# Kernel tuning notes

Hardware: AMD Instinct MI355X
Metric: run time of the kernel (lower is better)

## Reference

```python
import jax, jax.numpy as jnp
import numpy as np


def _binarize_ste(w):
    # forward: sign(w) in {-1, +1}; backward: identity (straight-through)
    wb = jnp.where(w >= 0, 1.0, -1.0).astype(w.dtype)
    return w + jax.lax.stop_gradient(wb - w)


def setup_inputs() -> dict:
    key = jax.random.key(0)
    k1, k2 = jax.random.split(key)
    IN, OUT, N = 2048, 2048, 8192
    x = jax.random.normal(k1, (N, IN), dtype=jnp.float32)
    # kaiming_uniform-like init: U(-bound, bound), bound = sqrt(6/in)*? (gain sqrt(5) default in torch)
    bound = float(np.sqrt(6.0 / IN))
    weight = jax.random.uniform(k2, (OUT, IN), dtype=jnp.float32, minval=-bound, maxval=bound)
    bias = jnp.zeros((OUT,), dtype=jnp.float32)
    return {"x": x, "weight": weight, "bias": bias}


def reference(x, weight, bias):
    w_binary = _binarize_ste(weight)  # [out, in], values in {-1, +1}
    # F.linear: x @ W^T + b
    return jnp.einsum('ni,oi->no', x, w_binary) + bias
```

## Files before the change

### kernel.cpp

```cpp
#include <hip/hip_runtime.h>
#include <stdint.h>


typedef __bf16 bf16x8 __attribute__((ext_vector_type(8)));
typedef float f32x16 __attribute__((ext_vector_type(16)));

typedef const __attribute__((address_space(1))) void* gas_ptr;
typedef __attribute__((address_space(3))) void* lds_ptr;

__device__ __forceinline__ unsigned short f2bf_rne(float f) {
    unsigned int u = __builtin_bit_cast(unsigned int, f);
    u += 0x7fffu + ((u >> 16) & 1u);
    return (unsigned short)(u >> 16);
}

__global__ __launch_bounds__(256) void cvt_x_kernel(const float* __restrict__ in,
                                                    unsigned short* __restrict__ out,
                                                    int n8) {
    int i = blockIdx.x * 256 + threadIdx.x;
    if (i >= n8) return;
    const float4* p = reinterpret_cast<const float4*>(in + (size_t)i * 8);
    float4 f0 = p[0], f1 = p[1];
    union { unsigned short s[8]; uint4 v; } o;
    o.s[0] = f2bf_rne(f0.x); o.s[1] = f2bf_rne(f0.y);
    o.s[2] = f2bf_rne(f0.z); o.s[3] = f2bf_rne(f0.w);
    o.s[4] = f2bf_rne(f1.x); o.s[5] = f2bf_rne(f1.y);
    o.s[6] = f2bf_rne(f1.z); o.s[7] = f2bf_rne(f1.w);
    *reinterpret_cast<uint4*>(out + (size_t)i * 8) = o.v;
}

__global__ __launch_bounds__(256) void bin_w_kernel(const float* __restrict__ in,
                                                    unsigned short* __restrict__ out,
                                                    int n4) {
    int i = blockIdx.x * 256 + threadIdx.x;
    if (i >= n4) return;
    float4 f = reinterpret_cast<const float4*>(in)[i];
    union { unsigned short s[4]; uint2 v; } o;
    o.s[0] = (f.x >= 0.f) ? 0x3F80u : 0xBF80u;
    o.s[1] = (f.y >= 0.f) ? 0x3F80u : 0xBF80u;
    o.s[2] = (f.z >= 0.f) ? 0x3F80u : 0xBF80u;
    o.s[3] = (f.w >= 0.f) ? 0x3F80u : 0xBF80u;
    reinterpret_cast<uint2*>(out)[i] = o.v;
}


#define WAITVM(N) asm volatile("s_waitcnt vmcnt(" #N ")" ::: "memory")

__device__ __forceinline__ void block_bar() {
    asm volatile("" ::: "memory");
    __builtin_amdgcn_s_barrier();
    asm volatile("" ::: "memory");
}

__global__ __launch_bounds__(512, 2) void gemm_bin_kernel(
    const unsigned short* __restrict__ A,
    const unsigned short* __restrict__ B,
    const float* __restrict__ bias,
    float* __restrict__ C,
    int M, int N, int K)
{
    __shared__ __align__(16) unsigned char smem_raw[131072];
    unsigned short* const sm = (unsigned short*)smem_raw;

    const int tid  = threadIdx.x;
    const int lane = tid & 63;
    const int wave = tid >> 6;
    const int wm   = wave >> 2;
    const int wn   = wave & 3;
    const int bm   = blockIdx.y;
    const int bn   = blockIdx.x;

    const unsigned short* __restrict__ Agb = A + (size_t)(bm * 256) * K;
    const unsigned short* __restrict__ Bgb = B + (size_t)(bn * 256) * K;

    const int lr = lane & 31;
    const int lk = lane >> 5;

    int offA[4][2], offB[2][2];
#pragma unroll
    for (int m = 0; m < 4; ++m) {
        const int r = wm * 128 + m * 32 + lr;
#pragma unroll
        for (int ks = 0; ks < 2; ++ks) {
            const int c = ks * 2 + lk;
            offA[m][ks] = (r * 4 + (c ^ ((r >> 1) & 3))) * 8;
        }
    }
#pragma unroll
    for (int n = 0; n < 2; ++n) {
        const int r = wn * 64 + n * 32 + lr;
#pragma unroll
        for (int ks = 0; ks < 2; ++ks) {
            const int c = ks * 2 + lk;
            offB[n][ks] = (r * 4 + (c ^ ((r >> 1) & 3))) * 8;
        }
    }

    int goff[2], lso[2];
#pragma unroll
    for (int j = 0; j < 2; ++j) {
        const int g = j * 512 + tid;
        const int r = g >> 2;
        const int c = (g & 3) ^ ((r >> 1) & 3);
        goff[j] = r * K + c * 8;
        lso[j]  = g * 8;
    }

    f32x16 acc[4][2];
#pragma unroll
    for (int m = 0; m < 4; ++m)
#pragma unroll
        for (int n = 0; n < 2; ++n)
#pragma unroll
            for (int r = 0; r < 16; ++r) acc[m][n][r] = 0.f;

    const int KT = K >> 5;

    auto stage = [&](int ts) {
        unsigned short* lA = sm + (ts & 3) * 16384;
        unsigned short* lB = lA + 8192;
        const unsigned short* ga = Agb + (size_t)ts * 32;
        const unsigned short* gb = Bgb + (size_t)ts * 32;
        __builtin_amdgcn_global_load_lds((gas_ptr)(ga + goff[0]), (lds_ptr)(lA + lso[0]), 16, 0, 0);
        __builtin_amdgcn_global_load_lds((gas_ptr)(ga + goff[1]), (lds_ptr)(lA + lso[1]), 16, 0, 0);
        __builtin_amdgcn_global_load_lds((gas_ptr)(gb + goff[0]), (lds_ptr)(lB + lso[0]), 16, 0, 0);
        __builtin_amdgcn_global_load_lds((gas_ptr)(gb + goff[1]), (lds_ptr)(lB + lso[1]), 16, 0, 0);
    };

    auto compute = [&](int t) {
        const unsigned short* lA = sm + (t & 3) * 16384;
        const unsigned short* lB = lA + 8192;
        bf16x8 af[4][2], bf[2][2];
#pragma unroll
        for (int m = 0; m < 4; ++m)
#pragma unroll
            for (int ks = 0; ks < 2; ++ks)
                af[m][ks] = *reinterpret_cast<const bf16x8*>(lA + offA[m][ks]);
#pragma unroll
        for (int n = 0; n < 2; ++n)
#pragma unroll
            for (int ks = 0; ks < 2; ++ks)
                bf[n][ks] = *reinterpret_cast<const bf16x8*>(lB + offB[n][ks]);
        __builtin_amdgcn_s_setprio(1);
#pragma unroll
        for (int ks = 0; ks < 2; ++ks)
#pragma unroll
            for (int m = 0; m < 4; ++m)
#pragma unroll
                for (int n = 0; n < 2; ++n)
                    acc[m][n] = __builtin_amdgcn_mfma_f32_32x32x16_bf16(
                        af[m][ks], bf[n][ks], acc[m][n], 0, 0, 0);
        __builtin_amdgcn_s_setprio(0);
    };

    stage(0); stage(1); stage(2);

    int t = 0;
    for (; t < KT - 3; ++t) {
        stage(t + 3);
        WAITVM(12);
        block_bar();
        compute(t);
        block_bar();
    }
    WAITVM(8);  block_bar(); compute(t); block_bar(); ++t;
    WAITVM(4);  block_bar(); compute(t); block_bar(); ++t;
    WAITVM(0);  block_bar(); compute(t);

    const int colb = bn * 256 + wn * 64;
    const float bv0 = bias[colb + lr];
    const float bv1 = bias[colb + 32 + lr];
    const int r0 = bm * 256 + wm * 128 + 4 * lk;
#pragma unroll
    for (int m = 0; m < 4; ++m)
#pragma unroll
        for (int n = 0; n < 2; ++n) {
            const float bvn = n ? bv1 : bv0;
            float* cp = C + (size_t)(r0 + m * 32) * N + colb + n * 32 + lr;
#pragma unroll
            for (int r = 0; r < 16; ++r) {
                const int rr = (r & 3) + 8 * (r >> 2);
                cp[(size_t)rr * N] = acc[m][n][r] + bvn;
            }
        }
}

extern "C" void kernel_launch(void* const* d_in, const int* in_sizes, int n_in,
                              void* d_out, int out_size, void* d_ws, size_t ws_size,
                              hipStream_t stream) {
    const float* x    = (const float*)d_in[0];
    const float* w    = (const float*)d_in[1];
    const float* bias = (const float*)d_in[2];
    float* out = (float*)d_out;

    const int K = 2048;
    const int N = in_sizes[2];
    const int M = in_sizes[0] / K;

    unsigned short* xb = (unsigned short*)d_ws;
    unsigned short* wb = xb + (size_t)M * K;

    const int nx8 = (M * K) / 8;
    const int nw4 = (N * K) / 4;
    cvt_x_kernel<<<(nx8 + 255) / 256, 256, 0, stream>>>(x, xb, nx8);
    bin_w_kernel<<<(nw4 + 255) / 256, 256, 0, stream>>>(w, wb, nw4);

    dim3 grid(N / 256, M / 256);
    gemm_bin_kernel<<<grid, 512, 0, stream>>>(xb, wb, bias, out, M, N, K);
}
```

Before: 201.3 us.

## Restructure GEMM main loop into four-phase ping-pong with interleaved staging

Replaces the 4-deep single-K-tile pipeline with a 64-wide K tile split into two 32-wide halves across double buffers. Each iteration runs four phases that each issue global-to-LDS loads for a future half-tile, read LDS fragments, sync, and run a batch of MFMAs, so memory traffic is spread across the compute. The bias load is hoisted before the loop. This adds more barriers per K step and more complex wait-count bookkeeping, which risks stalls or race bugs if the counts are wrong.

```diff
diff --git a/kernel.cpp b/kernel.cpp
--- a/kernel.cpp
+++ b/kernel.cpp
@@ -43,7 +43,6 @@
     reinterpret_cast<uint2*>(out)[i] = o.v;
 }
 
-
 #define WAITVM(N) asm volatile("s_waitcnt vmcnt(" #N ")" ::: "memory")
 
 __device__ __forceinline__ void block_bar() {
@@ -73,27 +72,32 @@
     const unsigned short* __restrict__ Agb = A + (size_t)(bm * 256) * K;
     const unsigned short* __restrict__ Bgb = B + (size_t)(bn * 256) * K;
 
-    const int lr = lane & 31;
-    const int lk = lane >> 5;
-
-    int offA[4][2], offB[2][2];
-#pragma unroll
-    for (int m = 0; m < 4; ++m) {
-        const int r = wm * 128 + m * 32 + lr;
-#pragma unroll
-        for (int ks = 0; ks < 2; ++ks) {
-            const int c = ks * 2 + lk;
-            offA[m][ks] = (r * 4 + (c ^ ((r >> 1) & 3))) * 8;
+    const int lr   = lane & 31;
+    const int lkhi = lane >> 5;
+
+    int offA[2][2][2][2];
+    int offB[2][2][2];
+#pragma unroll
+    for (int mh = 0; mh < 2; ++mh)
+#pragma unroll
+        for (int mi = 0; mi < 2; ++mi) {
+            const int r = wm * 128 + mh * 64 + mi * 32 + lr;
+            const int s = (r >> 1) & 3;
+#pragma unroll
+            for (int kh = 0; kh < 2; ++kh)
+#pragma unroll
+                for (int kk = 0; kk < 2; ++kk)
+                    offA[mh][mi][kh][kk] = kh * 8192 + (r * 4 + ((kk * 2 + lkhi) ^ s)) * 8;
         }
-    }
-#pragma unroll
-    for (int n = 0; n < 2; ++n) {
-        const int r = wn * 64 + n * 32 + lr;
-#pragma unroll
-        for (int ks = 0; ks < 2; ++ks) {
-            const int c = ks * 2 + lk;
-            offB[n][ks] = (r * 4 + (c ^ ((r >> 1) & 3))) * 8;
-        }
+#pragma unroll
+    for (int ni = 0; ni < 2; ++ni) {
+        const int r = wn * 64 + ni * 32 + lr;
+        const int s = (r >> 1) & 3;
+#pragma unroll
+        for (int kh = 0; kh < 2; ++kh)
+#pragma unroll
+            for (int kk = 0; kk < 2; ++kk)
+                offB[ni][kh][kk] = 16384 + kh * 8192 + (r * 4 + ((kk * 2 + lkhi) ^ s)) * 8;
     }
 
     int goff[2], lso[2];
@@ -106,6 +110,11 @@
         lso[j]  = g * 8;
     }
 
+    const int colb = bn * 256 + wn * 64;
+    float bv0 = bias[colb + lr];
+    float bv1 = bias[colb + 32 + lr];
+    asm volatile("" :: "v"(bv0), "v"(bv1));
+
     f32x16 acc[4][2];
 #pragma unroll
     for (int m = 0; m < 4; ++m)
@@ -114,63 +123,92 @@
 #pragma unroll
             for (int r = 0; r < 16; ++r) acc[m][n][r] = 0.f;
 
-    const int KT = K >> 5;
-
-    auto stage = [&](int ts) {
-        unsigned short* lA = sm + (ts & 3) * 16384;
-        unsigned short* lB = lA + 8192;
-        const unsigned short* ga = Agb + (size_t)ts * 32;
-        const unsigned short* gb = Bgb + (size_t)ts * 32;
-        __builtin_amdgcn_global_load_lds((gas_ptr)(ga + goff[0]), (lds_ptr)(lA + lso[0]), 16, 0, 0);
-        __builtin_amdgcn_global_load_lds((gas_ptr)(ga + goff[1]), (lds_ptr)(lA + lso[1]), 16, 0, 0);
-        __builtin_amdgcn_global_load_lds((gas_ptr)(gb + goff[0]), (lds_ptr)(lB + lso[0]), 16, 0, 0);
-        __builtin_amdgcn_global_load_lds((gas_ptr)(gb + goff[1]), (lds_ptr)(lB + lso[1]), 16, 0, 0);
+    bf16x8 bfr[2][2];
+
+    auto stage2 = [&](const unsigned short* gsrc, int ldsoff) {
+#pragma unroll
+        for (int j = 0; j < 2; ++j)
+            __builtin_amdgcn_global_load_lds((gas_ptr)(gsrc + goff[j]),
+                                             (lds_ptr)(sm + ldsoff + lso[j]), 16, 0, 0);
     };
 
-    auto compute = [&](int t) {
-        const unsigned short* lA = sm + (t & 3) * 16384;
-        const unsigned short* lB = lA + 8192;
-        bf16x8 af[4][2], bf[2][2];
-#pragma unroll
-        for (int m = 0; m < 4; ++m)
-#pragma unroll
-            for (int ks = 0; ks < 2; ++ks)
-                af[m][ks] = *reinterpret_cast<const bf16x8*>(lA + offA[m][ks]);
-#pragma unroll
-        for (int n = 0; n < 2; ++n)
-#pragma unroll
-            for (int ks = 0; ks < 2; ++ks)
-                bf[n][ks] = *reinterpret_cast<const bf16x8*>(lB + offB[n][ks]);
+    auto phase = [&](int bb, int mh, int kh, int readB,
+                     const unsigned short* gsrc, int ldsoff, int dostage) {
+        if (readB) {
+#pragma unroll
+            for (int ni = 0; ni < 2; ++ni)
+#pragma unroll
+                for (int kk = 0; kk < 2; ++kk)
+                    bfr[ni][kk] = *reinterpret_cast<const bf16x8*>(
+                        sm + bb + offB[ni][kh][kk]);
+        }
+        bf16x8 af[2][2];
+#pragma unroll
+        for (int mi = 0; mi < 2; ++mi)
+#pragma unroll
+            for (int kk = 0; kk < 2; ++kk)
+                af[mi][kk] = *reinterpret_cast<const bf16x8*>(
+                    sm + bb + offA[mh][mi][kh][kk]);
+        if (dostage) stage2(gsrc, ldsoff);
+        block_bar();
+        asm volatile("s_waitcnt lgkmcnt(0)" ::: "memory");
+        __builtin_amdgcn_sched_barrier(0);
         __builtin_amdgcn_s_setprio(1);
 #pragma unroll
-        for (int ks = 0; ks < 2; ++ks)
-#pragma unroll
-            for (int m = 0; m < 4; ++m)
-#pragma unroll
-                for (int n = 0; n < 2; ++n)
-                    acc[m][n] = __builtin_amdgcn_mfma_f32_32x32x16_bf16(
-                        af[m][ks], bf[n][ks], acc[m][n], 0, 0, 0);
+        for (int kk = 0; kk < 2; ++kk)
+#pragma unroll
+            for (int mi = 0; mi < 2; ++mi)
+#pragma unroll
+                for (int ni = 0; ni < 2; ++ni)
+                    acc[mh * 2 + mi][ni] = __builtin_amdgcn_mfma_f32_32x32x16_bf16(
+                        af[mi][kk], bfr[ni][kk], acc[mh * 2 + mi][ni], 0, 0, 0);
+        __builtin_amdgcn_sched_barrier(0);
         __builtin_amdgcn_s_setprio(0);
     };
 
-    stage(0); stage(1); stage(2);
-
-    int t = 0;
-    for (; t < KT - 3; ++t) {
-        stage(t + 3);
-        WAITVM(12);
-        block_bar();
-        compute(t);
-        block_bar();
-    }
-    WAITVM(8);  block_bar(); compute(t); block_bar(); ++t;
-    WAITVM(4);  block_bar(); compute(t); block_bar(); ++t;
-    WAITVM(0);  block_bar(); compute(t);
-
-    const int colb = bn * 256 + wn * 64;
-    const float bv0 = bias[colb + lr];
-    const float bv1 = bias[colb + 32 + lr];
-    const int r0 = bm * 256 + wm * 128 + 4 * lk;
+    const int KT = K >> 6;
+
+    stage2(Agb,      0);
+    stage2(Bgb,      16384);
+    stage2(Agb + 32, 8192);
+    stage2(Bgb + 32, 24576);
+    stage2(Agb + 64, 32768);
+    stage2(Bgb + 64, 32768 + 16384);
+    WAITVM(8);
+    block_bar();
+
+    for (int T = 0; T < KT - 2; ++T) {
+        const int bb = (T & 1) << 15;
+        const int nb = bb ^ 32768;
+        const unsigned short* gA1 = Agb + (size_t)(T + 1) * 64 + 32;
+        const unsigned short* gB1 = Bgb + (size_t)(T + 1) * 64 + 32;
+        const unsigned short* gA0 = Agb + (size_t)(T + 2) * 64;
+        const unsigned short* gB0 = Bgb + (size_t)(T + 2) * 64;
+        phase(bb, 0, 0, 1, gA1, nb + 8192,  1);            block_bar();
+        phase(bb, 1, 0, 0, gB1, nb + 24576, 1); WAITVM(8); block_bar();
+        phase(bb, 0, 1, 1, gA0, bb,         1);            block_bar();
+        phase(bb, 1, 1, 0, gB0, bb + 16384, 1); WAITVM(8); block_bar();
+    }
+    {
+        const int bb = ((KT - 2) & 1) << 15;
+        const int nb = bb ^ 32768;
+        const unsigned short* gA1 = Agb + (size_t)(KT - 1) * 64 + 32;
+        const unsigned short* gB1 = Bgb + (size_t)(KT - 1) * 64 + 32;
+        phase(bb, 0, 0, 1, gA1, nb + 8192,  1);            block_bar();
+        phase(bb, 1, 0, 0, gB1, nb + 24576, 1); WAITVM(8); block_bar();
+        phase(bb, 0, 1, 1, Agb, 0,          0);            block_bar();
+        phase(bb, 1, 1, 0, Agb, 0,          0); WAITVM(4); block_bar();
+    }
+    {
+        const int bb = ((KT - 1) & 1) << 15;
+        phase(bb, 0, 0, 1, Agb, 0, 0);                     block_bar();
+        phase(bb, 1, 0, 0, Agb, 0, 0);          WAITVM(0); block_bar();
+        phase(bb, 0, 1, 1, Agb, 0, 0);                     block_bar();
+        phase(bb, 1, 1, 0, Agb, 0, 0);
+    }
+
+    const float* bvp = bias;  (void)bvp;
+    const int r0 = bm * 256 + wm * 128 + 4 * lkhi;
 #pragma unroll
     for (int m = 0; m < 4; ++m)
 #pragma unroll
```

Result: faster. 193.4 us (-3.9%).

## Restructure bf16 GEMM main loop to 16x16x32 MFMA with double-buffered K=64 tiles

Applied to the files above, without the earlier changes.

Replaces the 32x32x16 MFMA tiling with 16x16x32 MFMAs (8x4 fragments per wave) and changes the LDS staging from a 4-deep ring of K=32 tiles to a double buffer of K=64 tiles with a new swizzle. The next tile's global-to-LDS loads are issued at the start of each K step and waited on at its end. Each K step is split into four M-subphases separated by block barriers, with explicit lgkmcnt waits and sched barriers around the MFMA bursts. The aim is fewer loop iterations and a different LDS access pattern, but it brings more barriers per step and shallower prefetch than the 3-ahead pipeline it replaces.

```diff
diff --git a/kernel.cpp b/kernel.cpp
--- a/kernel.cpp
+++ b/kernel.cpp
@@ -3,7 +3,7 @@
 
 
 typedef __bf16 bf16x8 __attribute__((ext_vector_type(8)));
-typedef float f32x16 __attribute__((ext_vector_type(16)));
+typedef float f32x4 __attribute__((ext_vector_type(4)));
 
 typedef const __attribute__((address_space(1))) void* gas_ptr;
 typedef __attribute__((address_space(3))) void* lds_ptr;
@@ -43,7 +43,6 @@
     reinterpret_cast<uint2*>(out)[i] = o.v;
 }
 
-
 #define WAITVM(N) asm volatile("s_waitcnt vmcnt(" #N ")" ::: "memory")
 
 __device__ __forceinline__ void block_bar() {
@@ -73,115 +72,118 @@
     const unsigned short* __restrict__ Agb = A + (size_t)(bm * 256) * K;
     const unsigned short* __restrict__ Bgb = B + (size_t)(bn * 256) * K;
 
-    const int lr = lane & 31;
-    const int lk = lane >> 5;
-
-    int offA[4][2], offB[2][2];
-#pragma unroll
-    for (int m = 0; m < 4; ++m) {
-        const int r = wm * 128 + m * 32 + lr;
-#pragma unroll
-        for (int ks = 0; ks < 2; ++ks) {
-            const int c = ks * 2 + lk;
-            offA[m][ks] = (r * 4 + (c ^ ((r >> 1) & 3))) * 8;
+    const int r15 = lane & 15;
+    const int kc  = lane >> 4;
+    const int sw  = ((r15 >> 2) & 1) << 1;
+
+    const int baseA0 = wm * 8192 + r15 * 64 + ((kc    ) ^ sw) * 8;
+    const int baseA1 = wm * 8192 + r15 * 64 + ((kc + 4) ^ sw) * 8;
+    const int bBq    = 16384 + (wn >> 1) * 8192 + (wn & 1) * 4096 + r15 * 64;
+    const int baseB0 = bBq + ((kc    ) ^ sw) * 8;
+    const int baseB1 = bBq + ((kc + 4) ^ sw) * 8;
+
+    int gsoff[2], ldoff[2];
+#pragma unroll
+    for (int j = 0; j < 2; ++j) {
+        const int g  = j * 512 + tid;
+        const int rl = g >> 3;
+        const int c  = (g & 7) ^ (((rl >> 2) & 1) << 1);
+        gsoff[j] = rl * K + c * 8;
+        ldoff[j] = g * 8;
+    }
+
+    const int colb = bn * 256 + wn * 64;
+    float bv[4];
+#pragma unroll
+    for (int nf = 0; nf < 4; ++nf) {
+        bv[nf] = bias[colb + nf * 16 + r15];
+        asm volatile("" :: "v"(bv[nf]));
+    }
+
+    f32x4 acc[8][4];
+#pragma unroll
+    for (int m = 0; m < 8; ++m)
+#pragma unroll
+        for (int n = 0; n < 4; ++n)
+#pragma unroll
+            for (int r = 0; r < 4; ++r) acc[m][n][r] = 0.f;
+
+    bf16x8 bfr[4][2];
+
+    auto stageAll = [&](int T1, unsigned short* dst) {
+        const unsigned short* ga = Agb + (size_t)T1 * 64;
+        const unsigned short* gb = Bgb + (size_t)T1 * 64;
+#pragma unroll
+        for (int j = 0; j < 2; ++j)
+            __builtin_amdgcn_global_load_lds((gas_ptr)(ga + gsoff[j]),
+                                             (lds_ptr)(dst + ldoff[j]), 16, 0, 0);
+#pragma unroll
+        for (int j = 0; j < 2; ++j)
+            __builtin_amdgcn_global_load_lds((gas_ptr)(ga + (size_t)128 * K + gsoff[j]),
+                                             (lds_ptr)(dst + 8192 + ldoff[j]), 16, 0, 0);
+#pragma unroll
+        for (int j = 0; j < 2; ++j)
+            __builtin_amdgcn_global_load_lds((gas_ptr)(gb + gsoff[j]),
+                                             (lds_ptr)(dst + 16384 + ldoff[j]), 16, 0, 0);
+#pragma unroll
+        for (int j = 0; j < 2; ++j)
+            __builtin_amdgcn_global_load_lds((gas_ptr)(gb + (size_t)128 * K + gsoff[j]),
+                                             (lds_ptr)(dst + 24576 + ldoff[j]), 16, 0, 0);
+    };
+
+    const int KT = K >> 6;
+
+    stageAll(0, sm);
+    WAITVM(0);
+    block_bar();
+
+    for (int T = 0; T < KT; ++T) {
+        const unsigned short* bb = sm + (T & 1) * 32768;
+        unsigned short* nb = sm + ((T + 1) & 1) * 32768;
+#pragma unroll
+        for (int mh = 0; mh < 4; ++mh) {
+            if (mh == 0) {
+                if (T + 1 < KT) stageAll(T + 1, nb);
+#pragma unroll
+                for (int nf = 0; nf < 4; ++nf) {
+                    bfr[nf][0] = *reinterpret_cast<const bf16x8*>(bb + baseB0 + nf * 1024);
+                    bfr[nf][1] = *reinterpret_cast<const bf16x8*>(bb + baseB1 + nf * 1024);
+                }
+            }
+            bf16x8 af[2][2];
+#pragma unroll
+            for (int mi = 0; mi < 2; ++mi) {
+                af[mi][0] = *reinterpret_cast<const bf16x8*>(bb + baseA0 + (mh * 2 + mi) * 1024);
+                af[mi][1] = *reinterpret_cast<const bf16x8*>(bb + baseA1 + (mh * 2 + mi) * 1024);
+            }
+            block_bar();
+            asm volatile("s_waitcnt lgkmcnt(0)" ::: "memory");
+            __builtin_amdgcn_sched_barrier(0);
+            __builtin_amdgcn_s_setprio(1);
+#pragma unroll
+            for (int kk = 0; kk < 2; ++kk)
+#pragma unroll
+                for (int mi = 0; mi < 2; ++mi)
+#pragma unroll
+                    for (int nf = 0; nf < 4; ++nf)
+                        acc[mh * 2 + mi][nf] = __builtin_amdgcn_mfma_f32_16x16x32_bf16(
+                            af[mi][kk], bfr[nf][kk], acc[mh * 2 + mi][nf], 0, 0, 0);
+            __builtin_amdgcn_sched_barrier(0);
+            __builtin_amdgcn_s_setprio(0);
+            if (mh == 3) { WAITVM(0); }
+            block_bar();
         }
     }
-#pragma unroll
-    for (int n = 0; n < 2; ++n) {
-        const int r = wn * 64 + n * 32 + lr;
-#pragma unroll
-        for (int ks = 0; ks < 2; ++ks) {
-            const int c = ks * 2 + lk;
-            offB[n][ks] = (r * 4 + (c ^ ((r >> 1) & 3))) * 8;
-        }
-    }
-
-    int goff[2], lso[2];
-#pragma unroll
-    for (int j = 0; j < 2; ++j) {
-        const int g = j * 512 + tid;
-        const int r = g >> 2;
-        const int c = (g & 3) ^ ((r >> 1) & 3);
-        goff[j] = r * K + c * 8;
-        lso[j]  = g * 8;
-    }
-
-    f32x16 acc[4][2];
-#pragma unroll
-    for (int m = 0; m < 4; ++m)
-#pragma unroll
-        for (int n = 0; n < 2; ++n)
-#pragma unroll
-            for (int r = 0; r < 16; ++r) acc[m][n][r] = 0.f;
-
-    const int KT = K >> 5;
-
-    auto stage = [&](int ts) {
-        unsigned short* lA = sm + (ts & 3) * 16384;
-        unsigned short* lB = lA + 8192;
-        const unsigned short* ga = Agb + (size_t)ts * 32;
-        const unsigned short* gb = Bgb + (size_t)ts * 32;
-        __builtin_amdgcn_global_load_lds((gas_ptr)(ga + goff[0]), (lds_ptr)(lA + lso[0]), 16, 0, 0);
-        __builtin_amdgcn_global_load_lds((gas_ptr)(ga + goff[1]), (lds_ptr)(lA + lso[1]), 16, 0, 0);
-        __builtin_amdgcn_global_load_lds((gas_ptr)(gb + goff[0]), (lds_ptr)(lB + lso[0]), 16, 0, 0);
-        __builtin_amdgcn_global_load_lds((gas_ptr)(gb + goff[1]), (lds_ptr)(lB + lso[1]), 16, 0, 0);
-    };
-
-    auto compute = [&](int t) {
-        const unsigned short* lA = sm + (t & 3) * 16384;
-        const unsigned short* lB = lA + 8192;
-        bf16x8 af[4][2], bf[2][2];
-#pragma unroll
-        for (int m = 0; m < 4; ++m)
-#pragma unroll
-            for (int ks = 0; ks < 2; ++ks)
-                af[m][ks] = *reinterpret_cast<const bf16x8*>(lA + offA[m][ks]);
-#pragma unroll
-        for (int n = 0; n < 2; ++n)
-#pragma unroll
-            for (int ks = 0; ks < 2; ++ks)
-                bf[n][ks] = *reinterpret_cast<const bf16x8*>(lB + offB[n][ks]);
-        __builtin_amdgcn_s_setprio(1);
-#pragma unroll
-        for (int ks = 0; ks < 2; ++ks)
-#pragma unroll
-            for (int m = 0; m < 4; ++m)
-#pragma unroll
-                for (int n = 0; n < 2; ++n)
-                    acc[m][n] = __builtin_amdgcn_mfma_f32_32x32x16_bf16(
-                        af[m][ks], bf[n][ks], acc[m][n], 0, 0, 0);
-        __builtin_amdgcn_s_setprio(0);
-    };
-
-    stage(0); stage(1); stage(2);
-
-    int t = 0;
-    for (; t < KT - 3; ++t) {
-        stage(t + 3);
-        WAITVM(12);
-        block_bar();
-        compute(t);
-        block_bar();
-    }
-    WAITVM(8);  block_bar(); compute(t); block_bar(); ++t;
-    WAITVM(4);  block_bar(); compute(t); block_bar(); ++t;
-    WAITVM(0);  block_bar(); compute(t);
-
-    const int colb = bn * 256 + wn * 64;
-    const float bv0 = bias[colb + lr];
-    const float bv1 = bias[colb + 32 + lr];
-    const int r0 = bm * 256 + wm * 128 + 4 * lk;
-#pragma unroll
-    for (int m = 0; m < 4; ++m)
-#pragma unroll
-        for (int n = 0; n < 2; ++n) {
-            const float bvn = n ? bv1 : bv0;
-            float* cp = C + (size_t)(r0 + m * 32) * N + colb + n * 32 + lr;
-#pragma unroll
-            for (int r = 0; r < 16; ++r) {
-                const int rr = (r & 3) + 8 * (r >> 2);
-                cp[(size_t)rr * N] = acc[m][n][r] + bvn;
-            }
+
+    const int row0 = bm * 256 + wm * 128 + kc * 4;
+#pragma unroll
+    for (int mf = 0; mf < 8; ++mf)
+#pragma unroll
+        for (int nf = 0; nf < 4; ++nf) {
+            float* cp = C + (size_t)(row0 + mf * 16) * N + colb + nf * 16 + r15;
+#pragma unroll
+            for (int r = 0; r < 4; ++r)
+                cp[(size_t)r * N] = acc[mf][nf][r] + bv[nf];
         }
 }
 
```

Measured after the change: 198.9 us. No clear change (-1.2%).
